# Kernel optimization log

Measured on AMD Instinct MI355X. Metric: run time of the kernel, lower is better.

## Reference

```python
import jax, jax.numpy as jnp
from jax import lax
import numpy as np


def conv2d(x, w, b, stride=1, pad=0):
    # x: [B,C,H,W], w: [O,I,kh,kw]
    y = lax.conv_general_dilated(
        x, w, (stride, stride), [(pad, pad), (pad, pad)],
        dimension_numbers=("NCHW", "OIHW", "NCHW"))
    return y + b[None, :, None, None]


def setup_inputs() -> dict:
    key = jax.random.key(0)
    ks = jax.random.split(key, 9)
    B, C, Ci, H, W = 1, 64, 32, 96, 96
    sc3 = 1.0 / np.sqrt(C * 9)   # fan-in scale for 3x3 convs
    sc1 = 1.0 / np.sqrt(C)       # fan-in scale for 1x1 convs
    scw = 1.0 / np.sqrt(Ci)
    return {
        "x":    jax.random.normal(ks[0], (B, C, H, W), jnp.float32),
        "d1_w": jax.random.normal(ks[1], (C, C, 3, 3), jnp.float32) * sc3,
        "d1_b": jnp.zeros((C,), jnp.float32),
        "d2_w": jax.random.normal(ks[2], (C, C, 3, 3), jnp.float32) * sc3,
        "d2_b": jnp.zeros((C,), jnp.float32),
        "d3_w": jax.random.normal(ks[3], (C, C, 3, 3), jnp.float32) * sc3,
        "d3_b": jnp.zeros((C,), jnp.float32),
        "g_w":  jax.random.normal(ks[4], (Ci, C, 1, 1), jnp.float32) * sc1,
        "g_b":  jnp.zeros((Ci,), jnp.float32),
        "th_w": jax.random.normal(ks[5], (Ci, C, 1, 1), jnp.float32) * sc1,
        "th_b": jnp.zeros((Ci,), jnp.float32),
        "ph_w": jax.random.normal(ks[6], (Ci, C, 1, 1), jnp.float32) * sc1,
        "ph_b": jnp.zeros((Ci,), jnp.float32),
        "W_w":  jax.random.normal(ks[7], (C, Ci, 1, 1), jnp.float32) * scw,
        "W_b":  jnp.zeros((C,), jnp.float32),
    }


def reference(x, d1_w, d1_b, d2_w, d2_b, d3_w, d3_b,
              g_w, g_b, th_w, th_b, ph_w, ph_b, W_w, W_b):
    lrelu = lambda v: jnp.where(v >= 0, v, 0.2 * v)
    y = lrelu(conv2d(x, d1_w, d1_b, stride=2, pad=1))
    y = lrelu(conv2d(y, d2_w, d2_b, stride=2, pad=1))
    y = conv2d(y, d3_w, d3_b, stride=2, pad=1)
    y = jax.image.resize(y, x.shape, method="bilinear")  # align_corners=False semantics
    x = jax.nn.sigmoid(y) * x
    # --- non-local block ---
    B, C, H, W = x.shape
    Ci = g_w.shape[0]
    gx = conv2d(x, g_w, g_b).reshape(B, Ci, -1)    # [B,Ci,N]
    tx = conv2d(x, th_w, th_b).reshape(B, Ci, -1)  # [B,Ci,N]
    px = conv2d(x, ph_w, ph_b).reshape(B, Ci, -1)  # [B,Ci,N]
    # f[b,n,m] = sum_c theta[b,n,c] * phi[b,c,m]  (N x N scores, no scaling)
    f = jnp.einsum("bcn,bcm->bnm", tx, px)
    f = jax.nn.softmax(f, axis=1)  # unconventional: softmax over FIRST token axis
    # y[b,c,n] = sum_m f[b,n,m] * g[b,c,m]
    y2 = jnp.einsum("bnm,bcm->bcn", f, gx).reshape(B, Ci, H, W)
    return conv2d(y2, W_w, W_b) + x
```

## Files before the change

kernel.cpp:

```cpp
#include <hip/hip_runtime.h>
#include <math.h>

#define NTOK 9216
#define CIN  32
#define CC   64
#define NCH1 16
#define NT1S 36
#define NCH2 12
#define MS2  24
#define LOG2E 1.4426950408889634f
#define C1INIT (-17.312340490667560f)
#define C2INIT (-9.3123404906675595f)

typedef _Float16 half8 __attribute__((ext_vector_type(8)));
typedef float    f32x4 __attribute__((ext_vector_type(4)));

static __device__ __forceinline__ float fexp2(float x) {
#if __has_builtin(__builtin_amdgcn_exp2f)
    return __builtin_amdgcn_exp2f(x);
#else
    return exp2f(x);
#endif
}

__global__ void conv3x3_quad96(const float* __restrict__ in, const float* __restrict__ w,
                               float* __restrict__ outp) {
    const int t = threadIdx.x;
    const int q = t % 12, ohl = t / 12;
    const int oh = blockIdx.x * 16 + ohl;
    const int oc = blockIdx.y, grp = blockIdx.z;
    const int ci0 = grp * 8;
    float a0 = 0.f, a1 = 0.f, a2 = 0.f, a3 = 0.f;
    const int iwl = 8 * q - 1;
    #pragma unroll
    for (int ci = 0; ci < 8; ++ci) {
        const float* ip = in + (ci0 + ci) * 96 * 96;
        const float* wp = w + oc * CC * 9 + (ci0 + ci) * 9;
        #pragma unroll
        for (int kh = 0; kh < 3; ++kh) {
            int ih = oh * 2 - 1 + kh;
            if (ih < 0) continue;
            const float* rp = ip + ih * 96;
            float ls = (q > 0) ? rp[iwl] : 0.f;
            float4 fa = *(const float4*)(rp + 8 * q);
            float4 fb = *(const float4*)(rp + 8 * q + 4);
            float w0 = wp[kh * 3], w1 = wp[kh * 3 + 1], w2 = wp[kh * 3 + 2];
            a0 = fmaf(ls,   w0, fmaf(fa.x, w1, fmaf(fa.y, w2, a0)));
            a1 = fmaf(fa.y, w0, fmaf(fa.z, w1, fmaf(fa.w, w2, a1)));
            a2 = fmaf(fa.w, w0, fmaf(fb.x, w1, fmaf(fb.y, w2, a2)));
            a3 = fmaf(fb.y, w0, fmaf(fb.z, w1, fmaf(fb.w, w2, a3)));
        }
    }
    float4 r = make_float4(a0, a1, a2, a3);
    *(float4*)(outp + grp * (CC * 2304) + oc * 2304 + oh * 48 + 4 * q) = r;
}

template<int HIN, int HOUT, int CIG>
__global__ void conv3x3_part(const float* __restrict__ in, const float* __restrict__ w,
                             float* __restrict__ outp) {
    const int p = blockIdx.x * blockDim.x + threadIdx.x;
    if (p >= HOUT * HOUT) return;
    const int oc = blockIdx.y, grp = blockIdx.z;
    const int oh = p / HOUT, ow = p % HOUT;
    const int ci0 = grp * CIG;
    float acc = 0.f;
    #pragma unroll
    for (int ci = 0; ci < CIG; ++ci) {
        const float* ip = in + (ci0 + ci) * HIN * HIN;
        const float* wp = w + oc * CC * 9 + (ci0 + ci) * 9;
        #pragma unroll
        for (int kh = 0; kh < 3; ++kh) {
            int ih = oh * 2 - 1 + kh;
            bool okh = (unsigned)ih < (unsigned)HIN;
            #pragma unroll
            for (int kw = 0; kw < 3; ++kw) {
                int iw = ow * 2 - 1 + kw;
                float v = (okh && (unsigned)iw < (unsigned)HIN) ? ip[ih * HIN + iw] : 0.f;
                acc = fmaf(v, wp[kh * 3 + kw], acc);
            }
        }
    }
    outp[grp * (CC * HOUT * HOUT) + oc * HOUT * HOUT + p] = acc;
}

template<int NG, int HW, int LRELU>
__global__ void conv_merge(const float* __restrict__ parts, const float* __restrict__ b,
                           float* __restrict__ out) {
    int idx = blockIdx.x * 256 + threadIdx.x;
    int oc = idx / HW;
    float acc = b[oc];
    #pragma unroll
    for (int g = 0; g < NG; ++g)
        acc += parts[g * (CC * HW) + idx];
    if (LRELU) acc = acc >= 0.f ? acc : 0.2f * acc;
    out[idx] = acc;
}

__global__ void gate_kernel(const float* __restrict__ x, const float* __restrict__ y3,
                            float* __restrict__ xg) {
    int idx = blockIdx.x * 256 + threadIdx.x;
    int c = idx / (96 * 96);
    int p = idx % (96 * 96);
    int h = p / 96, w = p % 96;
    float fh = (h + 0.5f) * 0.125f - 0.5f;
    float fw = (w + 0.5f) * 0.125f - 0.5f;
    int h0 = (int)floorf(fh); float ah = fh - (float)h0;
    int w0 = (int)floorf(fw); float aw = fw - (float)w0;
    int h0c = min(max(h0, 0), 11), h1c = min(max(h0 + 1, 0), 11);
    int w0c = min(max(w0, 0), 11), w1c = min(max(w0 + 1, 0), 11);
    const float* yp = y3 + c * 144;
    float v = (1.f - ah) * ((1.f - aw) * yp[h0c * 12 + w0c] + aw * yp[h0c * 12 + w1c])
            +         ah * ((1.f - aw) * yp[h1c * 12 + w0c] + aw * yp[h1c * 12 + w1c]);
    float sg = 1.f / (1.f + __expf(-v));
    xg[idx] = sg * x[idx];
}

__global__ void conv1x1_fused(const float* __restrict__ xg,
                              const float* __restrict__ gw, const float* __restrict__ gb,
                              const float* __restrict__ thw, const float* __restrict__ thb,
                              const float* __restrict__ phw, const float* __restrict__ phb,
                              float* __restrict__ gx, float* __restrict__ tx,
                              float* __restrict__ px) {
    int ci = blockIdx.y;
    int n = blockIdx.x * 256 + threadIdx.x;
    float ag = gb[ci], at = thb[ci], ap = phb[ci];
    #pragma unroll 8
    for (int c = 0; c < CC; ++c) {
        float v = xg[c * NTOK + n];
        ag = fmaf(gw[ci * CC + c],  v, ag);
        at = fmaf(thw[ci * CC + c], v, at);
        ap = fmaf(phw[ci * CC + c], v, ap);
    }
    gx[ci * NTOK + n] = ag;
    tx[ci * NTOK + n] = at * LOG2E;
    px[ci * NTOK + n] = ap;
}

__global__ void repackAB(const float* __restrict__ tx, const float* __restrict__ px,
                         _Float16* __restrict__ txF, _Float16* __restrict__ pxF) {
    const float* src = blockIdx.y ? px : tx;
    _Float16* dst    = blockIdx.y ? pxF : txF;
    int gid = blockIdx.x * 256 + threadIdx.x;
    int t = gid >> 6, l = gid & 63;
    int n = t * 16 + (l & 15);
    int khi = (l >> 4) * 4;
    half8 v;
    #pragma unroll
    for (int e = 0; e < 8; ++e) {
        int c = (e >> 2) * 16 + khi + (e & 3);
        v[e] = (_Float16)src[c * NTOK + n];
    }
    *(half8*)(dst + gid * 8) = v;
}

__global__ __launch_bounds__(256) void phase1(const _Float16* __restrict__ txF,
                                              const _Float16* __restrict__ pxF,
                                              float* __restrict__ Dp) {
    int w = threadIdx.x >> 6, l = threadIdx.x & 63;
    int mtile0 = (blockIdx.x * 4 + w) * 4;
    half8 pf[4];
    #pragma unroll
    for (int j = 0; j < 4; ++j)
        pf[j] = *(const half8*)(pxF + (mtile0 + j) * 512 + l * 8);
    f32x4 cini = {C1INIT, C1INIT, C1INIT, C1INIT};
    float dsum[4][4] = {};
    int nt0 = blockIdx.y * NT1S;
    for (int i = 0; i < NT1S; ++i) {
        half8 tf = *(const half8*)(txF + (nt0 + i) * 512 + l * 8);
        #pragma unroll
        for (int j = 0; j < 4; ++j) {
            f32x4 s = __builtin_amdgcn_mfma_f32_16x16x32_f16(pf[j], tf, cini, 0, 0, 0);
            #pragma unroll
            for (int r = 0; r < 4; ++r)
                dsum[j][r] += fexp2(s[r]);
        }
    }
    #pragma unroll
    for (int off = 1; off < 16; off <<= 1)
        #pragma unroll
        for (int j = 0; j < 4; ++j)
            #pragma unroll
            for (int r = 0; r < 4; ++r)
                dsum[j][r] += __shfl_xor(dsum[j][r], off);
    if ((l & 15) == 0) {
        #pragma unroll
        for (int j = 0; j < 4; ++j) {
            int m = (mtile0 + j) * 16 + (l >> 4) * 4;
            #pragma unroll
            for (int r = 0; r < 4; ++r)
                Dp[blockIdx.y * NTOK + m + r] = dsum[j][r];
        }
    }
}

__global__ void repackG(const float* __restrict__ gx, const float* __restrict__ Dp,
                        _Float16* __restrict__ gxF) {
    __shared__ float lds[CIN][65];
    __shared__ float idl[64];
    int m0 = blockIdx.x * 64;
    int tid = threadIdx.x;
    for (int idx = tid; idx < CIN * 64; idx += 256)
        lds[idx >> 6][idx & 63] = gx[(idx >> 6) * NTOK + m0 + (idx & 63)];
    if (tid < 64) {
        float D = 0.f;
        #pragma unroll
        for (int ch = 0; ch < NCH1; ++ch) D += Dp[ch * NTOK + m0 + tid];
        idl[tid] = 1.0f / D;
    }
    __syncthreads();
    int mt = tid >> 7;
    int slot = tid & 127;
    int ct = slot >> 6;
    int l  = slot & 63;
    int khi = (l >> 4) * 4;
    int c = ct * 16 + (l & 15);
    half8 v;
    #pragma unroll
    for (int e = 0; e < 8; ++e) {
        int mloc = mt * 32 + (e >> 2) * 16 + khi + (e & 3);
        v[e] = (_Float16)(lds[c][mloc] * idl[mloc]);
    }
    int tile = (blockIdx.x * 2 + mt) * 2 + ct;
    *(half8*)(gxF + tile * 512 + l * 8) = v;
}

__global__ __launch_bounds__(256) void phase2(const _Float16* __restrict__ txF,
                                              const _Float16* __restrict__ pxF,
                                              const _Float16* __restrict__ gxF,
                                              float* __restrict__ y2p) {
    int w = threadIdx.x >> 6, l = threadIdx.x & 63;
    int ntile0 = (blockIdx.x * 4 + w) * 4;
    half8 tf[4];
    #pragma unroll
    for (int j = 0; j < 4; ++j)
        tf[j] = *(const half8*)(txF + (ntile0 + j) * 512 + l * 8);
    int khi = (l >> 4) * 4;
    f32x4 zero = {0.f, 0.f, 0.f, 0.f};
    f32x4 cini = {C2INIT, C2INIT, C2INIT, C2INIT};
    f32x4 acc[4][2];
    #pragma unroll
    for (int j = 0; j < 4; ++j) { acc[j][0] = zero; acc[j][1] = zero; }
    int mbase = blockIdx.y * (NTOK / NCH2);
    for (int ms = 0; ms < MS2; ++ms) {
        int m0 = mbase + ms * 32;
        int mt16 = m0 >> 4;
        half8 pf0 = *(const half8*)(pxF + mt16 * 512 + l * 8);
        half8 pf1 = *(const half8*)(pxF + (mt16 + 1) * 512 + l * 8);
        int gt = (m0 >> 5) * 2;
        half8 gf0 = *(const half8*)(gxF + gt * 512 + l * 8);
        half8 gf1 = *(const half8*)(gxF + (gt + 1) * 512 + l * 8);
        #pragma unroll
        for (int j = 0; j < 4; ++j) {
            f32x4 s0 = __builtin_amdgcn_mfma_f32_16x16x32_f16(pf0, tf[j], cini, 0, 0, 0);
            f32x4 s1 = __builtin_amdgcn_mfma_f32_16x16x32_f16(pf1, tf[j], cini, 0, 0, 0);
            half8 ff;
            #pragma unroll
            for (int r = 0; r < 4; ++r) {
                ff[r]     = (_Float16)fexp2(s0[r]);
                ff[4 + r] = (_Float16)fexp2(s1[r]);
            }
            acc[j][0] = __builtin_amdgcn_mfma_f32_16x16x32_f16(ff, gf0, acc[j][0], 0, 0, 0);
            acc[j][1] = __builtin_amdgcn_mfma_f32_16x16x32_f16(ff, gf1, acc[j][1], 0, 0, 0);
        }
    }
    float* base = y2p + blockIdx.y * (CIN * NTOK);
    #pragma unroll
    for (int j = 0; j < 4; ++j) {
        int n = (ntile0 + j) * 16 + khi;
        #pragma unroll
        for (int r = 0; r < 4; ++r) {
            base[(l & 15) * NTOK + n + r]        = acc[j][0][r] * 0.00390625f;
            base[(16 + (l & 15)) * NTOK + n + r] = acc[j][1][r] * 0.00390625f;
        }
    }
}

__global__ void mergeY2(const float* __restrict__ y2p, float* __restrict__ att) {
    int idx = blockIdx.x * 256 + threadIdx.x;
    float s = 0.f;
    #pragma unroll
    for (int ch = 0; ch < NCH2; ++ch) s += y2p[ch * (CIN * NTOK) + idx];
    att[idx] = s;
}

__global__ void final_conv(const float* __restrict__ att, const float* __restrict__ Ww,
                           const float* __restrict__ Wb, const float* __restrict__ xg,
                           float* __restrict__ out) {
    int co = blockIdx.y;
    int n = blockIdx.x * 256 + threadIdx.x;
    float acc = Wb[co];
    #pragma unroll
    for (int ci = 0; ci < CIN; ++ci)
        acc = fmaf(Ww[co * CIN + ci], att[ci * NTOK + n], acc);
    out[co * NTOK + n] = acc + xg[co * NTOK + n];
}

extern "C" void kernel_launch(void* const* d_in, const int* in_sizes, int n_in,
                              void* d_out, int out_size, void* d_ws, size_t ws_size,
                              hipStream_t stream) {
    const float* x   = (const float*)d_in[0];
    const float* d1w = (const float*)d_in[1];  const float* d1b = (const float*)d_in[2];
    const float* d2w = (const float*)d_in[3];  const float* d2b = (const float*)d_in[4];
    const float* d3w = (const float*)d_in[5];  const float* d3b = (const float*)d_in[6];
    const float* gw  = (const float*)d_in[7];  const float* gb  = (const float*)d_in[8];
    const float* thw = (const float*)d_in[9];  const float* thb = (const float*)d_in[10];
    const float* phw = (const float*)d_in[11]; const float* phb = (const float*)d_in[12];
    const float* Ww  = (const float*)d_in[13]; const float* Wb  = (const float*)d_in[14];
    float* out = (float*)d_out;

    float* W    = (float*)d_ws;
    float* xg   = W;
    float* y1   = W + 589824;
    float* y2c  = W + 737280;
    float* y3   = W + 774144;
    float* txb  = W + 783360;
    float* pxb  = W + 1078272;
    float* gxb  = W + 1373184;
    float* Dp   = W + 1668096;
    float* att  = W + 1815552;
    float* y2p  = W + 2110464;
    _Float16* txF = (_Float16*)(W + 5649408);
    _Float16* pxF = (_Float16*)(W + 5796864);
    _Float16* gxF = (_Float16*)(W + 5944320);

    float* cp1 = y2p;
    float* cp2 = y2p + 1179648;
    float* cp3 = y2p + 1769472;

    conv3x3_quad96<<<dim3(3, CC, 8), 192, 0, stream>>>(x, d1w, cp1);
    conv_merge<8, 2304, 1><<<576, 256, 0, stream>>>(cp1, d1b, y1);
    conv3x3_part<48, 24, 4><<<dim3(3, CC, 16), 192, 0, stream>>>(y1,  d2w, cp2);
    conv_merge<16, 576, 1><<<144, 256, 0, stream>>>(cp2, d2b, y2c);
    conv3x3_part<24, 12, 4><<<dim3(1, CC, 16), 192, 0, stream>>>(y2c, d3w, cp3);
    conv_merge<16, 144, 0><<<36, 256, 0, stream>>>(cp3, d3b, y3);
    gate_kernel<<<2304, 256, 0, stream>>>(x, y3, xg);

    conv1x1_fused<<<dim3(36, CIN), 256, 0, stream>>>(xg, gw, gb, thw, thb, phw, phb,
                                                     gxb, txb, pxb);
    repackAB<<<dim3(144, 2), 256, 0, stream>>>(txb, pxb, txF, pxF);

    phase1<<<dim3(36, NCH1), 256, 0, stream>>>(txF, pxF, Dp);
    repackG<<<144, 256, 0, stream>>>(gxb, Dp, gxF);
    phase2<<<dim3(36, NCH2), 256, 0, stream>>>(txF, pxF, gxF, y2p);
    mergeY2<<<1152, 256, 0, stream>>>(y2p, att);

    final_conv<<<dim3(36, CC), 256, 0, stream>>>(att, Ww, Wb, xg, out);
}
```

Before: 122.3 us.

## Fuse gating, 1x1 projections and fp16 repack; fold softmax denominator into MFMA init

The gate, 1x1 projection and A/B/G fp16 repack kernels are merged into a single LDS-staged fused_proj kernel, so the gated x and fp32 projection intermediates are never written to global memory. The softmax column-normalisation moves from scaling G in repackG to subtracting log2(D) in the phase2 MFMA accumulator init, with a small mergeD kernel computing it. The first conv now computes two output channels per thread from a flattened grid, and the merge kernels use float4 accesses. The final conv recomputes the sigmoid gate from y3 instead of reading xg, trading some extra arithmetic for less memory traffic and fewer launches.

```diff
diff --git a/kernel.cpp b/kernel.cpp
--- a/kernel.cpp
+++ b/kernel.cpp
@@ -25,34 +25,44 @@
 
 __global__ void conv3x3_quad96(const float* __restrict__ in, const float* __restrict__ w,
                                float* __restrict__ outp) {
+    const int bid = blockIdx.x;
+    const int grp = bid & 7;
+    const int ocp = (bid >> 3) & 31;
+    const int bx  = bid >> 8;
     const int t = threadIdx.x;
     const int q = t % 12, ohl = t / 12;
-    const int oh = blockIdx.x * 16 + ohl;
-    const int oc = blockIdx.y, grp = blockIdx.z;
+    const int oh = bx * 16 + ohl;
     const int ci0 = grp * 8;
-    float a0 = 0.f, a1 = 0.f, a2 = 0.f, a3 = 0.f;
-    const int iwl = 8 * q - 1;
+    float a00 = 0.f, a01 = 0.f, a02 = 0.f, a03 = 0.f;
+    float a10 = 0.f, a11 = 0.f, a12 = 0.f, a13 = 0.f;
     #pragma unroll
     for (int ci = 0; ci < 8; ++ci) {
-        const float* ip = in + (ci0 + ci) * 96 * 96;
-        const float* wp = w + oc * CC * 9 + (ci0 + ci) * 9;
+        const float* ip = in + (ci0 + ci) * 9216;
+        const float* wp0 = w + (2 * ocp) * 576 + (ci0 + ci) * 9;
+        const float* wp1 = wp0 + 576;
         #pragma unroll
         for (int kh = 0; kh < 3; ++kh) {
             int ih = oh * 2 - 1 + kh;
             if (ih < 0) continue;
             const float* rp = ip + ih * 96;
-            float ls = (q > 0) ? rp[iwl] : 0.f;
+            float ls = (q > 0) ? rp[8 * q - 1] : 0.f;
             float4 fa = *(const float4*)(rp + 8 * q);
             float4 fb = *(const float4*)(rp + 8 * q + 4);
-            float w0 = wp[kh * 3], w1 = wp[kh * 3 + 1], w2 = wp[kh * 3 + 2];
-            a0 = fmaf(ls,   w0, fmaf(fa.x, w1, fmaf(fa.y, w2, a0)));
-            a1 = fmaf(fa.y, w0, fmaf(fa.z, w1, fmaf(fa.w, w2, a1)));
-            a2 = fmaf(fa.w, w0, fmaf(fb.x, w1, fmaf(fb.y, w2, a2)));
-            a3 = fmaf(fb.y, w0, fmaf(fb.z, w1, fmaf(fb.w, w2, a3)));
-        }
-    }
-    float4 r = make_float4(a0, a1, a2, a3);
-    *(float4*)(outp + grp * (CC * 2304) + oc * 2304 + oh * 48 + 4 * q) = r;
+            float w00 = wp0[kh * 3], w01 = wp0[kh * 3 + 1], w02 = wp0[kh * 3 + 2];
+            float w10 = wp1[kh * 3], w11 = wp1[kh * 3 + 1], w12 = wp1[kh * 3 + 2];
+            a00 = fmaf(ls,   w00, fmaf(fa.x, w01, fmaf(fa.y, w02, a00)));
+            a01 = fmaf(fa.y, w00, fmaf(fa.z, w01, fmaf(fa.w, w02, a01)));
+            a02 = fmaf(fa.w, w00, fmaf(fb.x, w01, fmaf(fb.y, w02, a02)));
+            a03 = fmaf(fb.y, w00, fmaf(fb.z, w01, fmaf(fb.w, w02, a03)));
+            a10 = fmaf(ls,   w10, fmaf(fa.x, w11, fmaf(fa.y, w12, a10)));
+            a11 = fmaf(fa.y, w10, fmaf(fa.z, w11, fmaf(fa.w, w12, a11)));
+            a12 = fmaf(fa.w, w10, fmaf(fb.x, w11, fmaf(fb.y, w12, a12)));
+            a13 = fmaf(fb.y, w10, fmaf(fb.z, w11, fmaf(fb.w, w12, a13)));
+        }
+    }
+    float* op = outp + grp * (CC * 2304) + (2 * ocp) * 2304 + oh * 48 + 4 * q;
+    *(float4*)op          = make_float4(a00, a01, a02, a03);
+    *(float4*)(op + 2304) = make_float4(a10, a11, a12, a13);
 }
 
 template<int HIN, int HOUT, int CIG>
@@ -84,73 +94,109 @@
 }
 
 template<int NG, int HW, int LRELU>
-__global__ void conv_merge(const float* __restrict__ parts, const float* __restrict__ b,
-                           float* __restrict__ out) {
-    int idx = blockIdx.x * 256 + threadIdx.x;
-    int oc = idx / HW;
-    float acc = b[oc];
-    #pragma unroll
-    for (int g = 0; g < NG; ++g)
-        acc += parts[g * (CC * HW) + idx];
-    if (LRELU) acc = acc >= 0.f ? acc : 0.2f * acc;
-    out[idx] = acc;
-}
-
-__global__ void gate_kernel(const float* __restrict__ x, const float* __restrict__ y3,
-                            float* __restrict__ xg) {
-    int idx = blockIdx.x * 256 + threadIdx.x;
-    int c = idx / (96 * 96);
-    int p = idx % (96 * 96);
-    int h = p / 96, w = p % 96;
+__global__ void conv_merge4(const float* __restrict__ parts, const float* __restrict__ b,
+                            float* __restrict__ out) {
+    int i4 = blockIdx.x * 256 + threadIdx.x;
+    int oc = (i4 * 4) / HW;
+    float bb = b[oc];
+    float4 acc = make_float4(bb, bb, bb, bb);
+    #pragma unroll
+    for (int g = 0; g < NG; ++g) {
+        float4 p = *(const float4*)(parts + g * (CC * HW) + i4 * 4);
+        acc.x += p.x; acc.y += p.y; acc.z += p.z; acc.w += p.w;
+    }
+    if (LRELU) {
+        acc.x = acc.x >= 0.f ? acc.x : 0.2f * acc.x;
+        acc.y = acc.y >= 0.f ? acc.y : 0.2f * acc.y;
+        acc.z = acc.z >= 0.f ? acc.z : 0.2f * acc.z;
+        acc.w = acc.w >= 0.f ? acc.w : 0.2f * acc.w;
+    }
+    *(float4*)(out + i4 * 4) = acc;
+}
+
+static __device__ __forceinline__ float gate_val(const float* __restrict__ y3c, int n) {
+    int h = n / 96, wc = n % 96;
     float fh = (h + 0.5f) * 0.125f - 0.5f;
-    float fw = (w + 0.5f) * 0.125f - 0.5f;
+    float fw = (wc + 0.5f) * 0.125f - 0.5f;
     int h0 = (int)floorf(fh); float ah = fh - (float)h0;
     int w0 = (int)floorf(fw); float aw = fw - (float)w0;
     int h0c = min(max(h0, 0), 11), h1c = min(max(h0 + 1, 0), 11);
     int w0c = min(max(w0, 0), 11), w1c = min(max(w0 + 1, 0), 11);
-    const float* yp = y3 + c * 144;
-    float v = (1.f - ah) * ((1.f - aw) * yp[h0c * 12 + w0c] + aw * yp[h0c * 12 + w1c])
-            +         ah * ((1.f - aw) * yp[h1c * 12 + w0c] + aw * yp[h1c * 12 + w1c]);
-    float sg = 1.f / (1.f + __expf(-v));
-    xg[idx] = sg * x[idx];
-}
-
-__global__ void conv1x1_fused(const float* __restrict__ xg,
-                              const float* __restrict__ gw, const float* __restrict__ gb,
-                              const float* __restrict__ thw, const float* __restrict__ thb,
-                              const float* __restrict__ phw, const float* __restrict__ phb,
-                              float* __restrict__ gx, float* __restrict__ tx,
-                              float* __restrict__ px) {
-    int ci = blockIdx.y;
-    int n = blockIdx.x * 256 + threadIdx.x;
-    float ag = gb[ci], at = thb[ci], ap = phb[ci];
-    #pragma unroll 8
-    for (int c = 0; c < CC; ++c) {
-        float v = xg[c * NTOK + n];
-        ag = fmaf(gw[ci * CC + c],  v, ag);
-        at = fmaf(thw[ci * CC + c], v, at);
-        ap = fmaf(phw[ci * CC + c], v, ap);
-    }
-    gx[ci * NTOK + n] = ag;
-    tx[ci * NTOK + n] = at * LOG2E;
-    px[ci * NTOK + n] = ap;
-}
-
-__global__ void repackAB(const float* __restrict__ tx, const float* __restrict__ px,
-                         _Float16* __restrict__ txF, _Float16* __restrict__ pxF) {
-    const float* src = blockIdx.y ? px : tx;
-    _Float16* dst    = blockIdx.y ? pxF : txF;
-    int gid = blockIdx.x * 256 + threadIdx.x;
-    int t = gid >> 6, l = gid & 63;
-    int n = t * 16 + (l & 15);
-    int khi = (l >> 4) * 4;
-    half8 v;
-    #pragma unroll
-    for (int e = 0; e < 8; ++e) {
-        int c = (e >> 2) * 16 + khi + (e & 3);
-        v[e] = (_Float16)src[c * NTOK + n];
-    }
-    *(half8*)(dst + gid * 8) = v;
+    float v = (1.f - ah) * ((1.f - aw) * y3c[h0c * 12 + w0c] + aw * y3c[h0c * 12 + w1c])
+            +         ah * ((1.f - aw) * y3c[h1c * 12 + w0c] + aw * y3c[h1c * 12 + w1c]);
+    return 1.f / (1.f + __expf(-v));
+}
+
+__global__ __launch_bounds__(256) void fused_proj(
+    const float* __restrict__ x, const float* __restrict__ y3,
+    const float* __restrict__ gw, const float* __restrict__ gb,
+    const float* __restrict__ thw, const float* __restrict__ thb,
+    const float* __restrict__ phw, const float* __restrict__ phb,
+    _Float16* __restrict__ txF, _Float16* __restrict__ pxF, _Float16* __restrict__ gxF) {
+    __shared__ float xgl[64][64];
+    __shared__ _Float16 pr[3][32][66];
+    const int t = threadIdx.x;
+    const int n0 = blockIdx.x * 64;
+    for (int idx = t; idx < 64 * 64; idx += 256) {
+        int c = idx >> 6, nl = idx & 63;
+        int n = n0 + nl;
+        float sg = gate_val(y3 + c * 144, n);
+        xgl[c][nl] = sg * x[c * NTOK + n];
+    }
+    __syncthreads();
+    const int w = t >> 6, l = t & 63;
+    {
+        float ag[8], at[8], ap[8];
+        #pragma unroll
+        for (int j = 0; j < 8; ++j) {
+            int ci = w * 8 + j;
+            ag[j] = gb[ci]; at[j] = thb[ci]; ap[j] = phb[ci];
+        }
+        #pragma unroll 4
+        for (int c = 0; c < 64; ++c) {
+            float v = xgl[c][l];
+            #pragma unroll
+            for (int j = 0; j < 8; ++j) {
+                int ci = w * 8 + j;
+                ag[j] = fmaf(gw[ci * CC + c],  v, ag[j]);
+                at[j] = fmaf(thw[ci * CC + c], v, at[j]);
+                ap[j] = fmaf(phw[ci * CC + c], v, ap[j]);
+            }
+        }
+        #pragma unroll
+        for (int j = 0; j < 8; ++j) {
+            pr[0][w * 8 + j][l] = (_Float16)(at[j] * LOG2E);
+            pr[1][w * 8 + j][l] = (_Float16)ap[j];
+            pr[2][w * 8 + j][l] = (_Float16)ag[j];
+        }
+    }
+    __syncthreads();
+    const int khi = (l >> 4) * 4;
+    {
+        int tile = blockIdx.x * 4 + w;
+        int nl = w * 16 + (l & 15);
+        half8 vt, vp;
+        #pragma unroll
+        for (int e = 0; e < 8; ++e) {
+            int c = (e >> 2) * 16 + khi + (e & 3);
+            vt[e] = pr[0][c][nl];
+            vp[e] = pr[1][c][nl];
+        }
+        *(half8*)(txF + tile * 512 + l * 8) = vt;
+        *(half8*)(pxF + tile * 512 + l * 8) = vp;
+    }
+    {
+        int mt = w >> 1, ct = w & 1;
+        int c2 = ct * 16 + (l & 15);
+        half8 vg;
+        #pragma unroll
+        for (int e = 0; e < 8; ++e) {
+            int ml = mt * 32 + (e >> 2) * 16 + khi + (e & 3);
+            vg[e] = pr[2][c2][ml];
+        }
+        int gtile = (blockIdx.x * 2 + mt) * 2 + ct;
+        *(half8*)(gxF + gtile * 512 + l * 8) = vg;
+    }
 }
 
 __global__ __launch_bounds__(256) void phase1(const _Float16* __restrict__ txF,
@@ -193,40 +239,18 @@
     }
 }
 
-__global__ void repackG(const float* __restrict__ gx, const float* __restrict__ Dp,
-                        _Float16* __restrict__ gxF) {
-    __shared__ float lds[CIN][65];
-    __shared__ float idl[64];
-    int m0 = blockIdx.x * 64;
-    int tid = threadIdx.x;
-    for (int idx = tid; idx < CIN * 64; idx += 256)
-        lds[idx >> 6][idx & 63] = gx[(idx >> 6) * NTOK + m0 + (idx & 63)];
-    if (tid < 64) {
-        float D = 0.f;
-        #pragma unroll
-        for (int ch = 0; ch < NCH1; ++ch) D += Dp[ch * NTOK + m0 + tid];
-        idl[tid] = 1.0f / D;
-    }
-    __syncthreads();
-    int mt = tid >> 7;
-    int slot = tid & 127;
-    int ct = slot >> 6;
-    int l  = slot & 63;
-    int khi = (l >> 4) * 4;
-    int c = ct * 16 + (l & 15);
-    half8 v;
-    #pragma unroll
-    for (int e = 0; e < 8; ++e) {
-        int mloc = mt * 32 + (e >> 2) * 16 + khi + (e & 3);
-        v[e] = (_Float16)(lds[c][mloc] * idl[mloc]);
-    }
-    int tile = (blockIdx.x * 2 + mt) * 2 + ct;
-    *(half8*)(gxF + tile * 512 + l * 8) = v;
+__global__ void mergeD(const float* __restrict__ Dp, float* __restrict__ log2D) {
+    int m = blockIdx.x * 256 + threadIdx.x;
+    float D = 0.f;
+    #pragma unroll
+    for (int ch = 0; ch < NCH1; ++ch) D += Dp[ch * NTOK + m];
+    log2D[m] = __log2f(D);
 }
 
 __global__ __launch_bounds__(256) void phase2(const _Float16* __restrict__ txF,
                                               const _Float16* __restrict__ pxF,
                                               const _Float16* __restrict__ gxF,
+                                              const float* __restrict__ log2D,
                                               float* __restrict__ y2p) {
     int w = threadIdx.x >> 6, l = threadIdx.x & 63;
     int ntile0 = (blockIdx.x * 4 + w) * 4;
@@ -236,7 +260,7 @@
         tf[j] = *(const half8*)(txF + (ntile0 + j) * 512 + l * 8);
     int khi = (l >> 4) * 4;
     f32x4 zero = {0.f, 0.f, 0.f, 0.f};
-    f32x4 cini = {C2INIT, C2INIT, C2INIT, C2INIT};
+    f32x4 c2v = {C2INIT, C2INIT, C2INIT, C2INIT};
     f32x4 acc[4][2];
     #pragma unroll
     for (int j = 0; j < 4; ++j) { acc[j][0] = zero; acc[j][1] = zero; }
@@ -246,13 +270,17 @@
         int mt16 = m0 >> 4;
         half8 pf0 = *(const half8*)(pxF + mt16 * 512 + l * 8);
         half8 pf1 = *(const half8*)(pxF + (mt16 + 1) * 512 + l * 8);
+        f32x4 l2a = *(const f32x4*)(log2D + m0 + khi);
+        f32x4 l2b = *(const f32x4*)(log2D + m0 + 16 + khi);
+        f32x4 cini0 = c2v - l2a;
+        f32x4 cini1 = c2v - l2b;
         int gt = (m0 >> 5) * 2;
         half8 gf0 = *(const half8*)(gxF + gt * 512 + l * 8);
         half8 gf1 = *(const half8*)(gxF + (gt + 1) * 512 + l * 8);
         #pragma unroll
         for (int j = 0; j < 4; ++j) {
-            f32x4 s0 = __builtin_amdgcn_mfma_f32_16x16x32_f16(pf0, tf[j], cini, 0, 0, 0);
-            f32x4 s1 = __builtin_amdgcn_mfma_f32_16x16x32_f16(pf1, tf[j], cini, 0, 0, 0);
+            f32x4 s0 = __builtin_amdgcn_mfma_f32_16x16x32_f16(pf0, tf[j], cini0, 0, 0, 0);
+            f32x4 s1 = __builtin_amdgcn_mfma_f32_16x16x32_f16(pf1, tf[j], cini1, 0, 0, 0);
             half8 ff;
             #pragma unroll
             for (int r = 0; r < 4; ++r) {
@@ -276,23 +304,27 @@
 }
 
 __global__ void mergeY2(const float* __restrict__ y2p, float* __restrict__ att) {
-    int idx = blockIdx.x * 256 + threadIdx.x;
-    float s = 0.f;
-    #pragma unroll
-    for (int ch = 0; ch < NCH2; ++ch) s += y2p[ch * (CIN * NTOK) + idx];
-    att[idx] = s;
+    int i4 = blockIdx.x * 256 + threadIdx.x;
+    float4 s = make_float4(0.f, 0.f, 0.f, 0.f);
+    #pragma unroll
+    for (int ch = 0; ch < NCH2; ++ch) {
+        float4 p = *(const float4*)(y2p + ch * (CIN * NTOK) + i4 * 4);
+        s.x += p.x; s.y += p.y; s.z += p.z; s.w += p.w;
+    }
+    *(float4*)(att + i4 * 4) = s;
 }
 
 __global__ void final_conv(const float* __restrict__ att, const float* __restrict__ Ww,
-                           const float* __restrict__ Wb, const float* __restrict__ xg,
-                           float* __restrict__ out) {
+                           const float* __restrict__ Wb, const float* __restrict__ x,
+                           const float* __restrict__ y3, float* __restrict__ out) {
     int co = blockIdx.y;
     int n = blockIdx.x * 256 + threadIdx.x;
     float acc = Wb[co];
     #pragma unroll
     for (int ci = 0; ci < CIN; ++ci)
         acc = fmaf(Ww[co * CIN + ci], att[ci * NTOK + n], acc);
-    out[co * NTOK + n] = acc + xg[co * NTOK + n];
+    float sg = gate_val(y3 + co * 144, n);
+    out[co * NTOK + n] = acc + sg * x[co * NTOK + n];
 }
 
 extern "C" void kernel_launch(void* const* d_in, const int* in_sizes, int n_in,
@@ -308,41 +340,36 @@
     const float* Ww  = (const float*)d_in[13]; const float* Wb  = (const float*)d_in[14];
     float* out = (float*)d_out;
 
-    float* W    = (float*)d_ws;
-    float* xg   = W;
-    float* y1   = W + 589824;
-    float* y2c  = W + 737280;
-    float* y3   = W + 774144;
-    float* txb  = W + 783360;
-    float* pxb  = W + 1078272;
-    float* gxb  = W + 1373184;
-    float* Dp   = W + 1668096;
-    float* att  = W + 1815552;
-    float* y2p  = W + 2110464;
-    _Float16* txF = (_Float16*)(W + 5649408);
-    _Float16* pxF = (_Float16*)(W + 5796864);
-    _Float16* gxF = (_Float16*)(W + 5944320);
+    float* W     = (float*)d_ws;
+    float* y1    = W;
+    float* y2c   = W + 147456;
+    float* y3    = W + 184320;
+    float* Dp    = W + 193536;
+    float* log2D = W + 340992;
+    float* att   = W + 350208;
+    float* y2p   = W + 645120;
+    _Float16* txF = (_Float16*)(W + 4184064);
+    _Float16* pxF = (_Float16*)(W + 4331520);
+    _Float16* gxF = (_Float16*)(W + 4478976);
 
     float* cp1 = y2p;
     float* cp2 = y2p + 1179648;
     float* cp3 = y2p + 1769472;
 
-    conv3x3_quad96<<<dim3(3, CC, 8), 192, 0, stream>>>(x, d1w, cp1);
-    conv_merge<8, 2304, 1><<<576, 256, 0, stream>>>(cp1, d1b, y1);
-    conv3x3_part<48, 24, 4><<<dim3(3, CC, 16), 192, 0, stream>>>(y1,  d2w, cp2);
-    conv_merge<16, 576, 1><<<144, 256, 0, stream>>>(cp2, d2b, y2c);
+    conv3x3_quad96<<<768, 192, 0, stream>>>(x, d1w, cp1);
+    conv_merge4<8, 2304, 1><<<144, 256, 0, stream>>>(cp1, d1b, y1);
+    conv3x3_part<48, 24, 4><<<dim3(3, CC, 16), 192, 0, stream>>>(y1, d2w, cp2);
+    conv_merge4<16, 576, 1><<<36, 256, 0, stream>>>(cp2, d2b, y2c);
     conv3x3_part<24, 12, 4><<<dim3(1, CC, 16), 192, 0, stream>>>(y2c, d3w, cp3);
-    conv_merge<16, 144, 0><<<36, 256, 0, stream>>>(cp3, d3b, y3);
-    gate_kernel<<<2304, 256, 0, stream>>>(x, y3, xg);
-
-    conv1x1_fused<<<dim3(36, CIN), 256, 0, stream>>>(xg, gw, gb, thw, thb, phw, phb,
-                                                     gxb, txb, pxb);
-    repackAB<<<dim3(144, 2), 256, 0, stream>>>(txb, pxb, txF, pxF);
+    conv_merge4<16, 144, 0><<<9, 256, 0, stream>>>(cp3, d3b, y3);
+
+    fused_proj<<<144, 256, 0, stream>>>(x, y3, gw, gb, thw, thb, phw, phb,
+                                        txF, pxF, gxF);
 
     phase1<<<dim3(36, NCH1), 256, 0, stream>>>(txF, pxF, Dp);
-    repackG<<<144, 256, 0, stream>>>(gxb, Dp, gxF);
-    phase2<<<dim3(36, NCH2), 256, 0, stream>>>(txF, pxF, gxF, y2p);
-    mergeY2<<<1152, 256, 0, stream>>>(y2p, att);
-
-    final_conv<<<dim3(36, CC), 256, 0, stream>>>(att, Ww, Wb, xg, out);
-}
+    mergeD<<<36, 256, 0, stream>>>(Dp, log2D);
+    phase2<<<dim3(36, NCH2), 256, 0, stream>>>(txF, pxF, gxF, log2D, y2p);
+    mergeY2<<<288, 256, 0, stream>>>(y2p, att);
+
+    final_conv<<<dim3(36, CC), 256, 0, stream>>>(att, Ww, Wb, x, y3, out);
+}
```

Result: slower. 132.9 us (+8.7%).
